# Kernel optimization log

Hardware: AMD Instinct MI355X
Metric: run time of the kernel (lower is better)

## Reference

```python
import jax, jax.numpy as jnp
import numpy as np

N_NODES = 50000
N_EDGES = 800000
IN_DIM = 256
HID = 128
OUT = 128
LEAKY_SLOPE = 0.01


def setup_inputs() -> dict:
    key = jax.random.key(0)
    ks = jax.random.split(key, 12)
    s = 0.05
    return {
        "h": jax.random.normal(ks[0], (N_NODES, IN_DIM), dtype=jnp.float32),
        "src": jax.random.randint(ks[1], (N_EDGES,), 0, N_NODES, dtype=jnp.int32),
        "dst": jax.random.randint(ks[2], (N_EDGES,), 0, N_NODES, dtype=jnp.int32),
        "W1": jax.random.normal(ks[3], (HID, IN_DIM), dtype=jnp.float32) * s,
        "b1": jax.random.normal(ks[4], (HID,), dtype=jnp.float32) * s,
        "a1": jax.random.normal(ks[5], (2 * HID,), dtype=jnp.float32) * s,
        "ab1": jax.random.normal(ks[6], (), dtype=jnp.float32) * s,
        "W2": jax.random.normal(ks[7], (OUT, HID), dtype=jnp.float32) * s,
        "b2": jax.random.normal(ks[8], (OUT,), dtype=jnp.float32) * s,
        "a2": jax.random.normal(ks[9], (2 * OUT,), dtype=jnp.float32) * s,
        "ab2": jax.random.normal(ks[10], (), dtype=jnp.float32) * s,
    }


def gat_layer(h, src, dst, W, b, a, ab, n_nodes):
    # z = fc(h)
    z = h @ W.T + b                      # [N, D]
    D = z.shape[-1]
    zs = z[src]                           # [E, D] gather src features
    zd = z[dst]                           # [E, D] gather dst features
    # attn_fc(cat[zs, zd]) == zs @ a[:D] + zd @ a[D:] + ab
    e = zs @ a[:D] + zd @ a[D:] + ab      # [E]
    e = jnp.where(e > 0, e, LEAKY_SLOPE * e)  # leaky_relu, slope 0.01
    # segment softmax over edges grouped by destination node
    m = jax.ops.segment_max(e, dst, num_segments=n_nodes)   # [N]
    ex = jnp.exp(e - m[dst])                                  # [E]
    denom = jax.ops.segment_sum(ex, dst, num_segments=n_nodes)  # [N]
    alpha = ex / denom[dst]                                   # [E]
    # weighted scatter-sum of src features into dst nodes
    return jax.ops.segment_sum(alpha[:, None] * zs, dst, num_segments=n_nodes)


def reference(h, src, dst, W1, b1, a1, ab1, W2, b2, a2, ab2):
    n = h.shape[0]
    h1 = jax.nn.elu(gat_layer(h, src, dst, W1, b1, a1, ab1, n))
    h2 = jax.nn.elu(gat_layer(h1, src, dst, W2, b2, a2, ab2, n))
    return h2
```

## Files before the change

kernel.cpp:

```cpp
#include <hip/hip_runtime.h>
#include <hip/hip_bf16.h>

#define N_NODES 50000
#define N_EDGES 800000
#define IN_DIM  256
#define HID     128
#define LEAKY   0.01f

#define EDGE_BLOCKS  ((N_EDGES + 255) / 256)
#define NODE_WBLKS   (N_NODES / 4)
#define SCAN_BLOCKS  ((N_NODES + 255) / 256)
#define W1_ELEMS  (HID * IN_DIM)
#define W2_ELEMS  (HID * HID)

#define TM        96
#define FC_BLOCKS ((N_NODES + TM - 1) / TM)
#define LDA       72

typedef __attribute__((ext_vector_type(8))) short short8;
typedef __attribute__((ext_vector_type(4))) float f32x4;

__device__ __forceinline__ unsigned short f2bf(float x) {
    union { __hip_bfloat16 b; unsigned short u; } c;
    c.b = __float2bfloat16(x);
    return c.u;
}
__device__ __forceinline__ float bf2f(unsigned short u) {
    union { unsigned int u; float f; } c;
    c.u = ((unsigned int)u) << 16;
    return c.f;
}
__device__ __forceinline__ float2 bfu2(unsigned int u) {
    float2 r;
    r.x = bf2f((unsigned short)(u & 0xffff));
    r.y = bf2f((unsigned short)(u >> 16));
    return r;
}
__device__ __forceinline__ float lky(float x) { return x > 0.f ? x : LEAKY * x; }
__device__ __forceinline__ float rl_f(float v, int l) {
    return __int_as_float(__builtin_amdgcn_readlane(__float_as_int(v), l));
}


__global__ void hist_split(const int* __restrict__ dst, int* __restrict__ counts,
                           int* __restrict__ erank,
                           const float* __restrict__ W1, unsigned short* __restrict__ w1hi,
                           unsigned short* __restrict__ w1lo,
                           const float* __restrict__ W2, unsigned short* __restrict__ w2hi,
                           unsigned short* __restrict__ w2lo) {
    int i = blockIdx.x * 256 + threadIdx.x;
    if (i < N_EDGES) erank[i] = atomicAdd(&counts[dst[i]], 1);
    if (i < W1_ELEMS) {
        float x = W1[i];
        unsigned short h = f2bf(x);
        w1hi[i] = h;
        w1lo[i] = f2bf(x - bf2f(h));
    } else if (i < W1_ELEMS + W2_ELEMS) {
        int j = i - W1_ELEMS;
        float x = W2[j];
        unsigned short h = f2bf(x);
        w2hi[j] = h;
        w2lo[j] = f2bf(x - bf2f(h));
    }
}

__global__ void scan_block(const int* __restrict__ counts, int* __restrict__ offsets,
                           int* __restrict__ bsums) {
    __shared__ int sh[256];
    int tid = threadIdx.x;
    int i = blockIdx.x * 256 + tid;
    int v = (i < N_NODES) ? counts[i] : 0;
    sh[tid] = v;
    __syncthreads();
    for (int o = 1; o < 256; o <<= 1) {
        int t = (tid >= o) ? sh[tid - o] : 0;
        __syncthreads();
        sh[tid] += t;
        __syncthreads();
    }
    if (i < N_NODES) offsets[i] = sh[tid] - v;
    if (tid == 255) bsums[blockIdx.x] = sh[255];
}

__global__ void scan_add(int* __restrict__ offsets, const int* __restrict__ bsums) {
    __shared__ int sh[256];
    int tid = threadIdx.x;
    int b = blockIdx.x;
    sh[tid] = (tid < b) ? bsums[tid] : 0;
    __syncthreads();
    for (int o = 128; o > 0; o >>= 1) {
        if (tid < o) sh[tid] += sh[tid + o];
        __syncthreads();
    }
    int base = sh[0];
    int i = b * 256 + tid;
    if (i < N_NODES) offsets[i] += base;
    if (i == N_NODES) offsets[N_NODES] = N_EDGES;
}

__global__ void fill_kernel(const int* __restrict__ dst, const int* __restrict__ src,
                            const int* __restrict__ erank,
                            const int* __restrict__ offsets,
                            int* __restrict__ csr_src) {
    int i = blockIdx.x * 256 + threadIdx.x;
    if (i < N_EDGES) {
        int d = dst[i];
        int slot = offsets[d] + erank[i];
        __builtin_nontemporal_store(src[i], &csr_src[slot]);
    }
}


__device__ __forceinline__ void epi(const f32x4* accn, int lrow0, int m0, int q, int lane,
                                    const float* __restrict__ bias,
                                    const float* __restrict__ attn,
                                    unsigned short* __restrict__ Zb,
                                    float* __restrict__ sbuf) {
    int r = lane & 15;
    int lrowbase = lrow0 + (lane >> 4) * 4;
    float ps[4] = {0.f, 0.f, 0.f, 0.f};
    float pd[4] = {0.f, 0.f, 0.f, 0.f};
#pragma unroll
    for (int nt = 0; nt < 4; nt++) {
        int n = q * 64 + nt * 16 + r;
        float bn = bias[n];
        float aS = attn[n];
        float aD = attn[HID + n];
#pragma unroll
        for (int reg = 0; reg < 4; reg++) {
            float zv = accn[nt][reg] + bn;
            if (m0 + lrowbase + reg < N_NODES)
                Zb[(size_t)(m0 + lrowbase + reg) * HID + n] = f2bf(zv);
            ps[reg] += zv * aS;
            pd[reg] += zv * aD;
        }
    }
#pragma unroll
    for (int o = 1; o < 16; o <<= 1) {
#pragma unroll
        for (int reg = 0; reg < 4; reg++) {
            ps[reg] += __shfl_xor(ps[reg], o, 64);
            pd[reg] += __shfl_xor(pd[reg], o, 64);
        }
    }
    if (r == 0) {
#pragma unroll
        for (int reg = 0; reg < 4; reg++) {
            sbuf[q * 192 + lrowbase + reg] = ps[reg];
            sbuf[q * 192 + 96 + lrowbase + reg] = pd[reg];
        }
    }
}

__device__ __forceinline__ void score_combine(const float* __restrict__ sbuf, int tid, int m0,
                                              float* __restrict__ sS, float* __restrict__ sD) {
    if (tid < 96) {
        int gr = m0 + tid;
        if (gr < N_NODES) {
            sS[gr] = sbuf[tid] + sbuf[192 + tid];
            sD[gr] = sbuf[96 + tid] + sbuf[192 + 96 + tid];
        }
    }
}


__launch_bounds__(256)
__global__ void gemm_fc1(const float* __restrict__ A,
                         const unsigned short* __restrict__ Whi,
                         const unsigned short* __restrict__ Wlo,
                         const float* __restrict__ bias,
                         const float* __restrict__ attn,
                         unsigned short* __restrict__ Zb,
                         float* __restrict__ sS, float* __restrict__ sD) {
    __shared__ unsigned short Ah[TM * LDA];
    __shared__ unsigned short Al[TM * LDA];
    __shared__ unsigned short Bh[HID * LDA];
    __shared__ unsigned short Bl[HID * LDA];

    int tid  = threadIdx.x;
    int lane = tid & 63;
    int w    = tid >> 6;
    int q    = w & 1;
    int mh   = w >> 1;
    int m0   = blockIdx.x * TM;
    int r    = lane & 15;
    int koff = (lane >> 4) * 8;

    f32x4 acc[3][4];
#pragma unroll
    for (int s = 0; s < 3; s++)
#pragma unroll
        for (int nt = 0; nt < 4; nt++) acc[s][nt] = (f32x4){0.f, 0.f, 0.f, 0.f};

    for (int kc = 0; kc < IN_DIM / 64; kc++) {
        int k0 = kc * 64;
        __syncthreads();
#pragma unroll
        for (int j = 0; j < 6; j++) {
            int flat = j * 256 + tid;
            int row = flat >> 4;
            int c4 = (flat & 15) << 2;
            int gr = m0 + row;
            if (gr >= N_NODES) gr = N_NODES - 1;
            float4 v = *(const float4*)(A + (size_t)gr * IN_DIM + k0 + c4);
            unsigned short h0 = f2bf(v.x), h1 = f2bf(v.y), h2 = f2bf(v.z), h3 = f2bf(v.w);
            short4 hv = {(short)h0, (short)h1, (short)h2, (short)h3};
            short4 lv = {(short)f2bf(v.x - bf2f(h0)), (short)f2bf(v.y - bf2f(h1)),
                         (short)f2bf(v.z - bf2f(h2)), (short)f2bf(v.w - bf2f(h3))};
            *(short4*)&Ah[row * LDA + c4] = hv;
            *(short4*)&Al[row * LDA + c4] = lv;
        }
#pragma unroll
        for (int j = 0; j < 4; j++) {
            int flat = j * 256 + tid;
            int n = flat >> 3;
            int c8 = (flat & 7) << 3;
            *(short8*)&Bh[n * LDA + c8] = *(const short8*)(Whi + (size_t)n * IN_DIM + k0 + c8);
            *(short8*)&Bl[n * LDA + c8] = *(const short8*)(Wlo + (size_t)n * IN_DIM + k0 + c8);
        }
        __syncthreads();
#pragma unroll
        for (int ks = 0; ks < 2; ks++) {
            int kk = ks * 32 + koff;
            short8 ah[3], al[3], bh[4], bl[4];
#pragma unroll
            for (int s = 0; s < 3; s++) {
                int row = mh * 48 + s * 16 + r;
                ah[s] = *(const short8*)&Ah[row * LDA + kk];
                al[s] = *(const short8*)&Al[row * LDA + kk];
            }
#pragma unroll
            for (int nt = 0; nt < 4; nt++) {
                int n = q * 64 + nt * 16 + r;
                bh[nt] = *(const short8*)&Bh[n * LDA + kk];
                bl[nt] = *(const short8*)&Bl[n * LDA + kk];
            }
#pragma unroll
            for (int s = 0; s < 3; s++)
#pragma unroll
                for (int nt = 0; nt < 4; nt++) {
                    acc[s][nt] = __builtin_amdgcn_mfma_f32_16x16x32_bf16(ah[s], bh[nt], acc[s][nt], 0, 0, 0);
                    acc[s][nt] = __builtin_amdgcn_mfma_f32_16x16x32_bf16(al[s], bh[nt], acc[s][nt], 0, 0, 0);
                    acc[s][nt] = __builtin_amdgcn_mfma_f32_16x16x32_bf16(ah[s], bl[nt], acc[s][nt], 0, 0, 0);
                }
        }
    }
    __syncthreads();
    float* sbuf = (float*)Ah;
#pragma unroll
    for (int s = 0; s < 3; s++)
        epi(acc[s], mh * 48 + s * 16, m0, q, lane, bias, attn, Zb, sbuf);
    __syncthreads();
    score_combine(sbuf, tid, m0, sS, sD);
}


__launch_bounds__(256)
__global__ void gemm_fc2(const unsigned short* __restrict__ Abf,
                         const unsigned short* __restrict__ Whi,
                         const unsigned short* __restrict__ Wlo,
                         const float* __restrict__ bias,
                         const float* __restrict__ attn,
                         unsigned short* __restrict__ Zb,
                         float* __restrict__ sS, float* __restrict__ sD) {
    __shared__ unsigned short Ah[TM * LDA];
    __shared__ unsigned short Bh[HID * LDA];
    __shared__ unsigned short Bl[HID * LDA];

    int tid  = threadIdx.x;
    int lane = tid & 63;
    int w    = tid >> 6;
    int q    = w & 1;
    int mh   = w >> 1;
    int m0   = blockIdx.x * TM;
    int r    = lane & 15;
    int koff = (lane >> 4) * 8;

    f32x4 acc[3][4];
#pragma unroll
    for (int s = 0; s < 3; s++)
#pragma unroll
        for (int nt = 0; nt < 4; nt++) acc[s][nt] = (f32x4){0.f, 0.f, 0.f, 0.f};

    for (int kc = 0; kc < HID / 64; kc++) {
        int k0 = kc * 64;
        __syncthreads();
#pragma unroll
        for (int j = 0; j < 3; j++) {
            int flat = j * 256 + tid;
            int row = flat >> 3;
            int c8 = (flat & 7) << 3;
            int gr = m0 + row;
            if (gr >= N_NODES) gr = N_NODES - 1;
            *(short8*)&Ah[row * LDA + c8] = *(const short8*)(Abf + (size_t)gr * HID + k0 + c8);
        }
#pragma unroll
        for (int j = 0; j < 4; j++) {
            int flat = j * 256 + tid;
            int n = flat >> 3;
            int c8 = (flat & 7) << 3;
            *(short8*)&Bh[n * LDA + c8] = *(const short8*)(Whi + (size_t)n * HID + k0 + c8);
            *(short8*)&Bl[n * LDA + c8] = *(const short8*)(Wlo + (size_t)n * HID + k0 + c8);
        }
        __syncthreads();
#pragma unroll
        for (int ks = 0; ks < 2; ks++) {
            int kk = ks * 32 + koff;
            short8 ah[3], bh[4], bl[4];
#pragma unroll
            for (int s = 0; s < 3; s++) {
                int row = mh * 48 + s * 16 + r;
                ah[s] = *(const short8*)&Ah[row * LDA + kk];
            }
#pragma unroll
            for (int nt = 0; nt < 4; nt++) {
                int n = q * 64 + nt * 16 + r;
                bh[nt] = *(const short8*)&Bh[n * LDA + kk];
                bl[nt] = *(const short8*)&Bl[n * LDA + kk];
            }
#pragma unroll
            for (int s = 0; s < 3; s++)
#pragma unroll
                for (int nt = 0; nt < 4; nt++) {
                    acc[s][nt] = __builtin_amdgcn_mfma_f32_16x16x32_bf16(ah[s], bh[nt], acc[s][nt], 0, 0, 0);
                    acc[s][nt] = __builtin_amdgcn_mfma_f32_16x16x32_bf16(ah[s], bl[nt], acc[s][nt], 0, 0, 0);
                }
        }
    }
    __syncthreads();
    float* sbuf = (float*)Ah;
#pragma unroll
    for (int s = 0; s < 3; s++)
        epi(acc[s], mh * 48 + s * 16, m0, q, lane, bias, attn, Zb, sbuf);
    __syncthreads();
    score_combine(sbuf, tid, m0, sS, sD);
}


template <int OUT_BF>
__launch_bounds__(256)
__global__ void aggregate(const unsigned short* __restrict__ Zb,
                          const int* __restrict__ csr_src,
                          const int* __restrict__ offsets,
                          const float* __restrict__ sS,
                          const float* __restrict__ sD,
                          const float* __restrict__ ab,
                          unsigned short* __restrict__ OutBf,
                          float* __restrict__ OutF) {
    int v = blockIdx.x * 4 + (threadIdx.x >> 6);
    int lane = threadIdx.x & 63;
    int off = offsets[v];
    int deg = offsets[v + 1] - off;
    float sdv = sD[v] + ab[0];

    const unsigned int* Zrow = (const unsigned int*)Zb;
    float2 acc = {0.f, 0.f};

    if (deg <= 64) {
        bool act = lane < deg;
        int s_l = 0;
        float x = -3.0e38f;
        if (act) {
            s_l = csr_src[off + lane];
            x = lky(sS[s_l] + sdv);
        }
        float mx = x;
#pragma unroll
        for (int o = 32; o > 0; o >>= 1) mx = fmaxf(mx, __shfl_xor(mx, o, 64));
        float ex = act ? __expf(x - mx) : 0.f;
        float sum = ex;
#pragma unroll
        for (int o = 32; o > 0; o >>= 1) sum += __shfl_xor(sum, o, 64);
        float al_l = (deg > 0) ? ex / sum : 0.f;

        int t = 0;
        for (; t + 16 <= deg; t += 16) {
            int   s[16];
            float a[16];
            unsigned int rw[16];
#pragma unroll
            for (int j = 0; j < 16; j++) {
                s[j] = __builtin_amdgcn_readlane(s_l, t + j);
                a[j] = rl_f(al_l, t + j);
            }
#pragma unroll
            for (int j = 0; j < 16; j++)
                rw[j] = Zrow[(size_t)s[j] * (HID / 2) + lane];
#pragma unroll
            for (int j = 0; j < 16; j++) {
                float2 zz = bfu2(rw[j]);
                acc.x += a[j] * zz.x;
                acc.y += a[j] * zz.y;
            }
        }
        for (; t + 4 <= deg; t += 4) {
            int   s[4];
            float a[4];
            unsigned int rw[4];
#pragma unroll
            for (int j = 0; j < 4; j++) {
                s[j] = __builtin_amdgcn_readlane(s_l, t + j);
                a[j] = rl_f(al_l, t + j);
            }
#pragma unroll
            for (int j = 0; j < 4; j++)
                rw[j] = Zrow[(size_t)s[j] * (HID / 2) + lane];
#pragma unroll
            for (int j = 0; j < 4; j++) {
                float2 zz = bfu2(rw[j]);
                acc.x += a[j] * zz.x;
                acc.y += a[j] * zz.y;
            }
        }
        for (; t < deg; t++) {
            int sj = __builtin_amdgcn_readlane(s_l, t);
            float aj = rl_f(al_l, t);
            float2 zz = bfu2(Zrow[(size_t)sj * (HID / 2) + lane]);
            acc.x += aj * zz.x;
            acc.y += aj * zz.y;
        }
    } else {
        float mx = -3.0e38f;
        for (int t = lane; t < deg; t += 64) {
            int s = csr_src[off + t];
            mx = fmaxf(mx, lky(sS[s] + sdv));
        }
#pragma unroll
        for (int o = 32; o > 0; o >>= 1) mx = fmaxf(mx, __shfl_xor(mx, o, 64));
        float sum = 0.f;
        for (int t = lane; t < deg; t += 64) {
            int s = csr_src[off + t];
            sum += __expf(lky(sS[s] + sdv) - mx);
        }
#pragma unroll
        for (int o = 32; o > 0; o >>= 1) sum += __shfl_xor(sum, o, 64);
        float inv = 1.f / sum;
        for (int t = 0; t < deg; t++) {
            int s = csr_src[off + t];
            float al = __expf(lky(sS[s] + sdv) - mx) * inv;
            float2 zz = bfu2(Zrow[(size_t)s * (HID / 2) + lane]);
            acc.x += al * zz.x;
            acc.y += al * zz.y;
        }
    }

    acc.x = acc.x > 0.f ? acc.x : __expf(acc.x) - 1.f;
    acc.y = acc.y > 0.f ? acc.y : __expf(acc.y) - 1.f;

    if (OUT_BF) {
        ushort2 o2;
        o2.x = f2bf(acc.x);
        o2.y = f2bf(acc.y);
        *((ushort2*)(OutBf + (size_t)v * HID + lane * 2)) = o2;
    } else {
        float2 o2 = {acc.x, acc.y};
        *((float2*)(OutF + (size_t)v * HID + lane * 2)) = o2;
    }
}


extern "C" void kernel_launch(void* const* d_in, const int* in_sizes, int n_in,
                              void* d_out, int out_size, void* d_ws, size_t ws_size,
                              hipStream_t stream) {
    const float* h   = (const float*)d_in[0];
    const int*   src = (const int*)d_in[1];
    const int*   dst = (const int*)d_in[2];
    const float* W1  = (const float*)d_in[3];
    const float* b1  = (const float*)d_in[4];
    const float* a1  = (const float*)d_in[5];
    const float* ab1 = (const float*)d_in[6];
    const float* W2  = (const float*)d_in[7];
    const float* b2  = (const float*)d_in[8];
    const float* a2  = (const float*)d_in[9];
    const float* ab2 = (const float*)d_in[10];
    float* out = (float*)d_out;

    unsigned short* zb = (unsigned short*)d_ws;
    float* sS = (float*)(zb + (size_t)N_NODES * HID);
    float* sD = sS + N_NODES;
    int* counts  = (int*)(sD + N_NODES);
    int* offsets = counts + N_NODES;
    int* bsums   = offsets + N_NODES + 16;
    unsigned short* h1   = (unsigned short*)(bsums + 256);
    unsigned short* w1hi = h1 + (size_t)N_NODES * HID;
    unsigned short* w1lo = w1hi + W1_ELEMS;
    unsigned short* w2hi = w1lo + W1_ELEMS;
    unsigned short* w2lo = w2hi + W2_ELEMS;
    int* csr_src = (int*)(w2lo + W2_ELEMS);
    int* erank   = csr_src + N_EDGES;

    hipMemsetAsync(counts, 0, (size_t)N_NODES * sizeof(int), stream);

    hist_split<<<EDGE_BLOCKS, 256, 0, stream>>>(dst, counts, erank,
                                                W1, w1hi, w1lo, W2, w2hi, w2lo);
    scan_block<<<SCAN_BLOCKS, 256, 0, stream>>>(counts, offsets, bsums);
    scan_add<<<SCAN_BLOCKS, 256, 0, stream>>>(offsets, bsums);
    fill_kernel<<<EDGE_BLOCKS, 256, 0, stream>>>(dst, src, erank, offsets, csr_src);

    gemm_fc1<<<FC_BLOCKS, 256, 0, stream>>>(h, w1hi, w1lo, b1, a1, zb, sS, sD);
    aggregate<1><<<NODE_WBLKS, 256, 0, stream>>>(zb, csr_src, offsets, sS, sD, ab1, h1, nullptr);

    gemm_fc2<<<FC_BLOCKS, 256, 0, stream>>>(h1, w2hi, w2lo, b2, a2, zb, sS, sD);
    aggregate<0><<<NODE_WBLKS, 256, 0, stream>>>(zb, csr_src, offsets, sS, sD, ab2, nullptr, out);
}
```

Before: 282.6 us.

## Load GEMM operands directly from global into registers, dropping LDS staging

Measured after the change: 313.3 us. +10.9%, slower.

```diff
diff --git a/kernel.cpp b/kernel.cpp
--- a/kernel.cpp
+++ b/kernel.cpp
@@ -13,9 +13,8 @@
 #define W1_ELEMS  (HID * IN_DIM)
 #define W2_ELEMS  (HID * HID)
 
-#define TM        96
+#define TM        64
 #define FC_BLOCKS ((N_NODES + TM - 1) / TM)
-#define LDA       72
 
 typedef __attribute__((ext_vector_type(8))) short short8;
 typedef __attribute__((ext_vector_type(4))) float f32x4;
@@ -39,6 +38,17 @@
 __device__ __forceinline__ float lky(float x) { return x > 0.f ? x : LEAKY * x; }
 __device__ __forceinline__ float rl_f(float v, int l) {
     return __int_as_float(__builtin_amdgcn_readlane(__float_as_int(v), l));
+}
+
+__device__ __forceinline__ void cvt8(const float4 v0, const float4 v1,
+                                     short8& hi, short8& lo) {
+    float f[8] = {v0.x, v0.y, v0.z, v0.w, v1.x, v1.y, v1.z, v1.w};
+#pragma unroll
+    for (int j = 0; j < 8; j++) {
+        unsigned short h = f2bf(f[j]);
+        hi[j] = (short)h;
+        lo[j] = (short)f2bf(f[j] - bf2f(h));
+    }
 }
 
 
@@ -146,25 +156,25 @@
     if (r == 0) {
 #pragma unroll
         for (int reg = 0; reg < 4; reg++) {
-            sbuf[q * 192 + lrowbase + reg] = ps[reg];
-            sbuf[q * 192 + 96 + lrowbase + reg] = pd[reg];
+            sbuf[q * 128 + lrowbase + reg] = ps[reg];
+            sbuf[q * 128 + 64 + lrowbase + reg] = pd[reg];
         }
     }
 }
 
 __device__ __forceinline__ void score_combine(const float* __restrict__ sbuf, int tid, int m0,
                                               float* __restrict__ sS, float* __restrict__ sD) {
-    if (tid < 96) {
+    if (tid < TM) {
         int gr = m0 + tid;
         if (gr < N_NODES) {
-            sS[gr] = sbuf[tid] + sbuf[192 + tid];
-            sD[gr] = sbuf[96 + tid] + sbuf[192 + 96 + tid];
-        }
-    }
-}
-
-
-__launch_bounds__(256)
+            sS[gr] = sbuf[tid] + sbuf[128 + tid];
+            sD[gr] = sbuf[64 + tid] + sbuf[128 + 64 + tid];
+        }
+    }
+}
+
+
+__launch_bounds__(256, 3)
 __global__ void gemm_fc1(const float* __restrict__ A,
                          const unsigned short* __restrict__ Whi,
                          const unsigned short* __restrict__ Wlo,
@@ -172,10 +182,7 @@
                          const float* __restrict__ attn,
                          unsigned short* __restrict__ Zb,
                          float* __restrict__ sS, float* __restrict__ sD) {
-    __shared__ unsigned short Ah[TM * LDA];
-    __shared__ unsigned short Al[TM * LDA];
-    __shared__ unsigned short Bh[HID * LDA];
-    __shared__ unsigned short Bl[HID * LDA];
+    __shared__ float sbuf[256];
 
     int tid  = threadIdx.x;
     int lane = tid & 63;
@@ -186,76 +193,56 @@
     int r    = lane & 15;
     int koff = (lane >> 4) * 8;
 
-    f32x4 acc[3][4];
-#pragma unroll
-    for (int s = 0; s < 3; s++)
+    const float* Ap[2];
+#pragma unroll
+    for (int s = 0; s < 2; s++) {
+        int gr = m0 + mh * 32 + s * 16 + r;
+        if (gr >= N_NODES) gr = N_NODES - 1;
+        Ap[s] = A + (size_t)gr * IN_DIM + koff;
+    }
+    const unsigned short* Bph = Whi + (size_t)(q * 64 + r) * IN_DIM + koff;
+    const unsigned short* Bpl = Wlo + (size_t)(q * 64 + r) * IN_DIM + koff;
+
+    f32x4 acc[2][4];
+#pragma unroll
+    for (int s = 0; s < 2; s++)
 #pragma unroll
         for (int nt = 0; nt < 4; nt++) acc[s][nt] = (f32x4){0.f, 0.f, 0.f, 0.f};
 
-    for (int kc = 0; kc < IN_DIM / 64; kc++) {
-        int k0 = kc * 64;
-        __syncthreads();
-#pragma unroll
-        for (int j = 0; j < 6; j++) {
-            int flat = j * 256 + tid;
-            int row = flat >> 4;
-            int c4 = (flat & 15) << 2;
-            int gr = m0 + row;
-            if (gr >= N_NODES) gr = N_NODES - 1;
-            float4 v = *(const float4*)(A + (size_t)gr * IN_DIM + k0 + c4);
-            unsigned short h0 = f2bf(v.x), h1 = f2bf(v.y), h2 = f2bf(v.z), h3 = f2bf(v.w);
-            short4 hv = {(short)h0, (short)h1, (short)h2, (short)h3};
-            short4 lv = {(short)f2bf(v.x - bf2f(h0)), (short)f2bf(v.y - bf2f(h1)),
-                         (short)f2bf(v.z - bf2f(h2)), (short)f2bf(v.w - bf2f(h3))};
-            *(short4*)&Ah[row * LDA + c4] = hv;
-            *(short4*)&Al[row * LDA + c4] = lv;
-        }
-#pragma unroll
-        for (int j = 0; j < 4; j++) {
-            int flat = j * 256 + tid;
-            int n = flat >> 3;
-            int c8 = (flat & 7) << 3;
-            *(short8*)&Bh[n * LDA + c8] = *(const short8*)(Whi + (size_t)n * IN_DIM + k0 + c8);
-            *(short8*)&Bl[n * LDA + c8] = *(const short8*)(Wlo + (size_t)n * IN_DIM + k0 + c8);
-        }
-        __syncthreads();
-#pragma unroll
-        for (int ks = 0; ks < 2; ks++) {
-            int kk = ks * 32 + koff;
-            short8 ah[3], al[3], bh[4], bl[4];
-#pragma unroll
-            for (int s = 0; s < 3; s++) {
-                int row = mh * 48 + s * 16 + r;
-                ah[s] = *(const short8*)&Ah[row * LDA + kk];
-                al[s] = *(const short8*)&Al[row * LDA + kk];
-            }
+#pragma unroll 2
+    for (int kt = 0; kt < IN_DIM / 32; kt++) {
+        int k0 = kt * 32;
+        short8 ah[2], al[2], bh[4], bl[4];
+#pragma unroll
+        for (int nt = 0; nt < 4; nt++) {
+            bh[nt] = *(const short8*)(Bph + (size_t)nt * 16 * IN_DIM + k0);
+            bl[nt] = *(const short8*)(Bpl + (size_t)nt * 16 * IN_DIM + k0);
+        }
+#pragma unroll
+        for (int s = 0; s < 2; s++) {
+            float4 v0 = *(const float4*)(Ap[s] + k0);
+            float4 v1 = *(const float4*)(Ap[s] + k0 + 4);
+            cvt8(v0, v1, ah[s], al[s]);
+        }
+#pragma unroll
+        for (int s = 0; s < 2; s++)
 #pragma unroll
             for (int nt = 0; nt < 4; nt++) {
-                int n = q * 64 + nt * 16 + r;
-                bh[nt] = *(const short8*)&Bh[n * LDA + kk];
-                bl[nt] = *(const short8*)&Bl[n * LDA + kk];
-            }
-#pragma unroll
-            for (int s = 0; s < 3; s++)
-#pragma unroll
-                for (int nt = 0; nt < 4; nt++) {
-                    acc[s][nt] = __builtin_amdgcn_mfma_f32_16x16x32_bf16(ah[s], bh[nt], acc[s][nt], 0, 0, 0);
-                    acc[s][nt] = __builtin_amdgcn_mfma_f32_16x16x32_bf16(al[s], bh[nt], acc[s][nt], 0, 0, 0);
-                    acc[s][nt] = __builtin_amdgcn_mfma_f32_16x16x32_bf16(ah[s], bl[nt], acc[s][nt], 0, 0, 0);
-                }
-        }
-    }
-    __syncthreads();
-    float* sbuf = (float*)Ah;
-#pragma unroll
-    for (int s = 0; s < 3; s++)
-        epi(acc[s], mh * 48 + s * 16, m0, q, lane, bias, attn, Zb, sbuf);
+                acc[s][nt] = __builtin_amdgcn_mfma_f32_16x16x32_bf16(ah[s], bh[nt], acc[s][nt], 0, 0, 0);
+                acc[s][nt] = __builtin_amdgcn_mfma_f32_16x16x32_bf16(al[s], bh[nt], acc[s][nt], 0, 0, 0);
+                acc[s][nt] = __builtin_amdgcn_mfma_f32_16x16x32_bf16(ah[s], bl[nt], acc[s][nt], 0, 0, 0);
+            }
+    }
+
+#pragma unroll
+    for (int s = 0; s < 2; s++)
+        epi(acc[s], mh * 32 + s * 16, m0, q, lane, bias, attn, Zb, sbuf);
     __syncthreads();
     score_combine(sbuf, tid, m0, sS, sD);
 }
 
 
-__launch_bounds__(256)
+__launch_bounds__(256, 3)
 __global__ void gemm_fc2(const unsigned short* __restrict__ Abf,
                          const unsigned short* __restrict__ Whi,
                          const unsigned short* __restrict__ Wlo,
@@ -263,9 +250,7 @@
                          const float* __restrict__ attn,
                          unsigned short* __restrict__ Zb,
                          float* __restrict__ sS, float* __restrict__ sD) {
-    __shared__ unsigned short Ah[TM * LDA];
-    __shared__ unsigned short Bh[HID * LDA];
-    __shared__ unsigned short Bl[HID * LDA];
+    __shared__ float sbuf[256];
 
     int tid  = threadIdx.x;
     int lane = tid & 63;
@@ -276,62 +261,46 @@
     int r    = lane & 15;
     int koff = (lane >> 4) * 8;
 
-    f32x4 acc[3][4];
-#pragma unroll
-    for (int s = 0; s < 3; s++)
+    const unsigned short* Ap[2];
+#pragma unroll
+    for (int s = 0; s < 2; s++) {
+        int gr = m0 + mh * 32 + s * 16 + r;
+        if (gr >= N_NODES) gr = N_NODES - 1;
+        Ap[s] = Abf + (size_t)gr * HID + koff;
+    }
+    const unsigned short* Bph = Whi + (size_t)(q * 64 + r) * HID + koff;
+    const unsigned short* Bpl = Wlo + (size_t)(q * 64 + r) * HID + koff;
+
+    f32x4 acc[2][4];
+#pragma unroll
+    for (int s = 0; s < 2; s++)
 #pragma unroll
         for (int nt = 0; nt < 4; nt++) acc[s][nt] = (f32x4){0.f, 0.f, 0.f, 0.f};
 
-    for (int kc = 0; kc < HID / 64; kc++) {
-        int k0 = kc * 64;
-        __syncthreads();
-#pragma unroll
-        for (int j = 0; j < 3; j++) {
-            int flat = j * 256 + tid;
-            int row = flat >> 3;
-            int c8 = (flat & 7) << 3;
-            int gr = m0 + row;
-            if (gr >= N_NODES) gr = N_NODES - 1;
-            *(short8*)&Ah[row * LDA + c8] = *(const short8*)(Abf + (size_t)gr * HID + k0 + c8);
-        }
-#pragma unroll
-        for (int j = 0; j < 4; j++) {
-            int flat = j * 256 + tid;
-            int n = flat >> 3;
-            int c8 = (flat & 7) << 3;
-            *(short8*)&Bh[n * LDA + c8] = *(const short8*)(Whi + (size_t)n * HID + k0 + c8);
-            *(short8*)&Bl[n * LDA + c8] = *(const short8*)(Wlo + (size_t)n * HID + k0 + c8);
-        }
-        __syncthreads();
-#pragma unroll
-        for (int ks = 0; ks < 2; ks++) {
-            int kk = ks * 32 + koff;
-            short8 ah[3], bh[4], bl[4];
-#pragma unroll
-            for (int s = 0; s < 3; s++) {
-                int row = mh * 48 + s * 16 + r;
-                ah[s] = *(const short8*)&Ah[row * LDA + kk];
-            }
+#pragma unroll 2
+    for (int kt = 0; kt < HID / 32; kt++) {
+        int k0 = kt * 32;
+        short8 ah[2], bh[4], bl[4];
+#pragma unroll
+        for (int nt = 0; nt < 4; nt++) {
+            bh[nt] = *(const short8*)(Bph + (size_t)nt * 16 * HID + k0);
+            bl[nt] = *(const short8*)(Bpl + (size_t)nt * 16 * HID + k0);
+        }
+#pragma unroll
+        for (int s = 0; s < 2; s++)
+            ah[s] = *(const short8*)(Ap[s] + k0);
+#pragma unroll
+        for (int s = 0; s < 2; s++)
 #pragma unroll
             for (int nt = 0; nt < 4; nt++) {
-                int n = q * 64 + nt * 16 + r;
-                bh[nt] = *(const short8*)&Bh[n * LDA + kk];
-                bl[nt] = *(const short8*)&Bl[n * LDA + kk];
-            }
-#pragma unroll
-            for (int s = 0; s < 3; s++)
-#pragma unroll
-                for (int nt = 0; nt < 4; nt++) {
-                    acc[s][nt] = __builtin_amdgcn_mfma_f32_16x16x32_bf16(ah[s], bh[nt], acc[s][nt], 0, 0, 0);
-                    acc[s][nt] = __builtin_amdgcn_mfma_f32_16x16x32_bf16(ah[s], bl[nt], acc[s][nt], 0, 0, 0);
-                }
-        }
-    }
-    __syncthreads();
-    float* sbuf = (float*)Ah;
-#pragma unroll
-    for (int s = 0; s < 3; s++)
-        epi(acc[s], mh * 48 + s * 16, m0, q, lane, bias, attn, Zb, sbuf);
+                acc[s][nt] = __builtin_amdgcn_mfma_f32_16x16x32_bf16(ah[s], bh[nt], acc[s][nt], 0, 0, 0);
+                acc[s][nt] = __builtin_amdgcn_mfma_f32_16x16x32_bf16(ah[s], bl[nt], acc[s][nt], 0, 0, 0);
+            }
+    }
+
+#pragma unroll
+    for (int s = 0; s < 2; s++)
+        epi(acc[s], mh * 32 + s * 16, m0, q, lane, bias, attn, Zb, sbuf);
     __syncthreads();
     score_combine(sbuf, tid, m0, sS, sD);
 }
```
